# Performance work log

Hardware: AMD Instinct MI355X
Metric: run time of the kernel (lower is better)

## Reference

```python
import jax, jax.numpy as jnp
import numpy as np

B, C, N = 4, 256, 2048
H = 8
HD = C // H  # head_dim = 32


def setup_inputs() -> dict:
    key = jax.random.key(0)
    ks = jax.random.split(key, 5)
    s = 1.0 / np.sqrt(C)
    return {
        "x": jax.random.normal(ks[0], (B, C, 3, N), dtype=jnp.float32),
        "Wq": jax.random.normal(ks[1], (C, C), dtype=jnp.float32) * s,
        "Wk": jax.random.normal(ks[2], (C, C), dtype=jnp.float32) * s,
        "Wv": jax.random.normal(ks[3], (C, C), dtype=jnp.float32) * s,
        "Wo": jax.random.normal(ks[4], (C, C), dtype=jnp.float32) * s,
    }


def _vn_linear(W, x):
    # nn.Linear over channel axis: out[b,o,d,n] = sum_c W[o,c] x[b,c,d,n]
    return jnp.einsum('oc,bcdn->bodn', W, x)


def _heads(t):
    # [B,C,3,N] -> [B,H,N,HD,3]
    return t.reshape(B, H, HD, 3, N).transpose(0, 1, 4, 2, 3)


def reference(x, Wq, Wk, Wv, Wo):
    q = _heads(_vn_linear(Wq, x))
    k = _heads(_vn_linear(Wk, x))
    v = _heads(_vn_linear(Wv, x))
    # energy contracts over (head_dim, 3)
    energy = jnp.einsum('bhnci,bhmci->bhnm', q, k)
    attn = jax.nn.softmax(energy / np.sqrt(HD), axis=-1)
    out = jnp.einsum('bhnm,bhmci->bhnci', attn, v)
    # [B,H,N,HD,3] -> [B,C,3,N]
    out = out.transpose(0, 1, 3, 4, 2).reshape(B, C, 3, N)
    out = _vn_linear(Wo, out)
    return out + x
```

## Files before the change

kernel.cpp:

```cpp
#include <hip/hip_runtime.h>
#include <hip/hip_bf16.h>
#include <cmath>


typedef unsigned short u16;
typedef unsigned int   u32;
typedef u16   u16x8  __attribute__((ext_vector_type(8)));
typedef short s16x8  __attribute__((ext_vector_type(8)));
typedef float f32x4  __attribute__((ext_vector_type(4)));
typedef float f32x16 __attribute__((ext_vector_type(16)));

namespace {
constexpr int Nc = 2048, Fc = 96;
constexpr float SCALE_LOG2 = 0.17677669529663687f * 1.4426950408889634f;
constexpr int KP = 104;
constexpr int VP = 40;
constexpr int VOFF = 32 * KP;
constexpr int SBUF = VOFF + 96 * VP;
}

__device__ inline float fast_exp2(float x) {
#if __has_builtin(__builtin_amdgcn_exp2f)
    return __builtin_amdgcn_exp2f(x);
#else
    return exp2f(x);
#endif
}

__device__ inline u16 f2bf(float x) {
    union { float f; unsigned u; } v; v.f = x;
    unsigned r = v.u + 0x7FFFu + ((v.u >> 16) & 1u);
    return (u16)(r >> 16);
}

__device__ inline float bf2f(u16 x) {
    union { unsigned u; float f; } v; v.u = ((unsigned)x) << 16; return v.f;
}

__global__ __launch_bounds__(256) void wconv_kernel(
    const float* __restrict__ Wq, const float* __restrict__ Wk,
    const float* __restrict__ Wv, const float* __restrict__ Wo,
    u16* __restrict__ Wb)
{
    const int id = blockIdx.x * 256 + threadIdx.x;
    const int base = id * 8;
    const int o = base >> 8, c = base & 255;
    const int sel = o >> 8, ol = o & 255;
    const float* src = (sel == 0) ? Wq : (sel == 1) ? Wk : (sel == 2) ? Wv : Wo;
    const float sc = (sel == 0) ? SCALE_LOG2 : 1.0f;
    const float4 a = *(const float4*)&src[(size_t)ol * 256 + c];
    const float4 b = *(const float4*)&src[(size_t)ol * 256 + c + 4];
    u16x8 r;
    r[0]=f2bf(a.x*sc); r[1]=f2bf(a.y*sc); r[2]=f2bf(a.z*sc); r[3]=f2bf(a.w*sc);
    r[4]=f2bf(b.x*sc); r[5]=f2bf(b.y*sc); r[6]=f2bf(b.z*sc); r[7]=f2bf(b.w*sc);
    *(u16x8*)&Wb[(size_t)o * 256 + c] = r;
}

__global__ __launch_bounds__(256) void xt_kernel(
    const float* __restrict__ x, u16* __restrict__ xt)
{
    const int nt = blockIdx.x, ct = blockIdx.y, bi = blockIdx.z;
    const int b = bi / 3, i = bi % 3;
    const int t = (int)threadIdx.x;
    const int n0 = nt * 64, c0 = ct * 64;

    __shared__ u16 tile[64][72];

    const int n_l = t & 63;
#pragma unroll
    for (int it = 0; it < 16; ++it) {
        const int c_l = (t >> 6) + it * 4;
        tile[n_l][c_l] =
            f2bf(x[(((size_t)(b * 256 + c0 + c_l)) * 3 + i) * Nc + n0 + n_l]);
    }
    __syncthreads();
#pragma unroll
    for (int it = 0; it < 2; ++it) {
        const int idx = t + it * 256;
        const int nn = idx >> 3, part = idx & 7;
        *(u16x8*)&xt[((size_t)bi * Nc + n0 + nn) * 256 + c0 + part * 8] =
            *(const u16x8*)&tile[nn][part * 8];
    }
}

__global__ __launch_bounds__(256) void qkv_gemm_kernel(
    const u16* __restrict__ xt, const u16* __restrict__ wb,
    u16* __restrict__ Qt, u16* __restrict__ Kt, u16* __restrict__ Vf)
{
    const int nt = blockIdx.x;
    const int wy = blockIdx.y;
    const int bi = blockIdx.z;
    const int b = bi / 3, i = bi % 3;
    const int wsel = wy >> 1, ot = wy & 1;

    const u16* xs = xt + ((size_t)bi * Nc + nt * 128) * 256;
    const u16* ws = wb + (size_t)(wsel * 256 + ot * 128) * 256;

    __shared__ u16 xl[128][40];
    __shared__ u16 wl[128][40];

    const int t = (int)threadIdx.x;
    const int wv = t >> 6, lane = t & 63;
    const int g = lane >> 4, c16 = lane & 15;
    const int wr = wv >> 1, wc = wv & 1;

    f32x4 acc[4][4];
#pragma unroll
    for (int mi = 0; mi < 4; ++mi)
#pragma unroll
        for (int ni = 0; ni < 4; ++ni)
#pragma unroll
            for (int r = 0; r < 4; ++r) acc[mi][ni][r] = 0.f;

    for (int ks = 0; ks < 8; ++ks) {
        __syncthreads();
#pragma unroll
        for (int it = 0; it < 2; ++it) {
            const int idx = t + it * 256;
            const int row = idx >> 2, part = idx & 3;
            *(u16x8*)&xl[row][part * 8] =
                *(const u16x8*)&xs[(size_t)row * 256 + ks * 32 + part * 8];
            *(u16x8*)&wl[row][part * 8] =
                *(const u16x8*)&ws[(size_t)row * 256 + ks * 32 + part * 8];
        }
        __syncthreads();

        s16x8 af[4], bf[4];
        if (wsel < 2) {
#pragma unroll
            for (int mi = 0; mi < 4; ++mi) af[mi] = *(const s16x8*)&xl[wr*64 + mi*16 + c16][g*8];
#pragma unroll
            for (int ni = 0; ni < 4; ++ni) bf[ni] = *(const s16x8*)&wl[wc*64 + ni*16 + c16][g*8];
        } else {
#pragma unroll
            for (int mi = 0; mi < 4; ++mi) af[mi] = *(const s16x8*)&wl[wr*64 + mi*16 + c16][g*8];
#pragma unroll
            for (int ni = 0; ni < 4; ++ni) bf[ni] = *(const s16x8*)&xl[wc*64 + ni*16 + c16][g*8];
        }
#pragma unroll
        for (int mi = 0; mi < 4; ++mi)
#pragma unroll
            for (int ni = 0; ni < 4; ++ni)
                acc[mi][ni] = __builtin_amdgcn_mfma_f32_16x16x32_bf16(
                    af[mi], bf[ni], acc[mi][ni], 0, 0, 0);
    }

    if (wsel < 2) {
        u16* dst = wsel ? Kt : Qt;
#pragma unroll
        for (int mi = 0; mi < 4; ++mi)
#pragma unroll
            for (int ni = 0; ni < 4; ++ni) {
                const int o = ot * 128 + wc * 64 + ni * 16 + c16;
                const int h = o >> 5, cw = o & 31;
#pragma unroll
                for (int r = 0; r < 4; ++r) {
                    const int n = nt * 128 + wr * 64 + mi * 16 + g * 4 + r;
                    dst[((size_t)(b * 8 + h) * Nc + n) * Fc + i * 32 + cw] =
                        f2bf(acc[mi][ni][r]);
                }
            }
    } else {
#pragma unroll
        for (int mi = 0; mi < 4; ++mi)
#pragma unroll
            for (int ni = 0; ni < 4; ++ni) {
                const int n = nt * 128 + wc * 64 + ni * 16 + c16;
#pragma unroll
                for (int r = 0; r < 4; ++r) {
                    const int o = ot * 128 + wr * 64 + mi * 16 + g * 4 + r;
                    const int h = o >> 5, cw = o & 31;
                    Vf[((size_t)(b * 8 + h) * Fc + i * 32 + cw) * Nc + n] =
                        f2bf(acc[mi][ni][r]);
                }
            }
    }
}

__global__ __launch_bounds__(256) void attn_mfma_kernel(
    const u16* __restrict__ Qt, const u16* __restrict__ Kt,
    const u16* __restrict__ Vf, u16* __restrict__ Ob, float* __restrict__ lP)
{
    const int bid = (int)blockIdx.x;
    const int lid = (bid & 7) * 128 + (bid >> 3);
    const int bh   = lid >> 5;
    const int r5   = lid & 31;
    const int qt   = r5 >> 1;
    const int half = r5 & 1;

    const int t_   = (int)threadIdx.x;
    const int wq   = t_ >> 6;
    const int lane = t_ & 63;
    const int ql   = lane & 31;
    const int hi   = lane >> 5;

    __shared__ u16 sbuf[2 * SBUF];

    const int qb = qt * 128 + wq * 32;
    const int k0 = half * 1024;

    s16x8 bq[6];
#pragma unroll
    for (int s6 = 0; s6 < 6; ++s6)
        bq[s6] = *(const s16x8*)&Qt[((size_t)bh * Nc + qb + ql) * Fc + s6 * 16 + hi * 8];

    const u16* g_cur[3]; int g_str[3], g_dst[3];
#pragma unroll
    for (int it = 0; it < 3; ++it) {
        const int c = t_ + it * 256;
        if (c < 384) {
            const int row = c / 12, part = c - row * 12;
            g_cur[it] = Kt + ((size_t)bh * Nc + k0 + row) * Fc + part * 8;
            g_str[it] = 32 * Fc;
            g_dst[it] = row * KP + part * 8;
        } else {
            const int c2 = c - 384, f = c2 >> 2, part = c2 & 3;
            g_cur[it] = Vf + ((size_t)bh * Fc + f) * Nc + k0 + part * 8;
            g_str[it] = 32;
            g_dst[it] = VOFF + f * VP + part * 8;
        }
    }

    f32x16 acc[3];
#pragma unroll
    for (int ft = 0; ft < 3; ++ft)
#pragma unroll
        for (int r = 0; r < 16; ++r) acc[ft][r] = 0.f;
    float lacc[8];
#pragma unroll
    for (int r = 0; r < 8; ++r) lacc[r] = 0.f;

    u16* bA = sbuf;
    u16* bB = sbuf + SBUF;

    u16x8 sreg[3];
#pragma unroll
    for (int it = 0; it < 3; ++it) { sreg[it] = *(const u16x8*)g_cur[it]; g_cur[it] += g_str[it]; }
#pragma unroll
    for (int it = 0; it < 3; ++it) *(u16x8*)&bA[g_dst[it]] = sreg[it];
#pragma unroll
    for (int it = 0; it < 3; ++it) { sreg[it] = *(const u16x8*)g_cur[it]; g_cur[it] += g_str[it]; }
    __syncthreads();

    for (int kt = 0; kt < 32; ++kt) {
        if (kt < 31) {
#pragma unroll
            for (int it = 0; it < 3; ++it) *(u16x8*)&bB[g_dst[it]] = sreg[it];
        }
        if (kt < 30) {
#pragma unroll
            for (int it = 0; it < 3; ++it) { sreg[it] = *(const u16x8*)g_cur[it]; g_cur[it] += g_str[it]; }
        }

        f32x16 sv;
#pragma unroll
        for (int r = 0; r < 16; ++r) sv[r] = 0.f;
#pragma unroll
        for (int s6 = 0; s6 < 6; ++s6) {
            const s16x8 ka = *(const s16x8*)&bA[ql * KP + s6 * 16 + hi * 8];
            sv = __builtin_amdgcn_mfma_f32_32x32x16_bf16(ka, bq[s6], sv, 0, 0, 0);
        }

#pragma unroll
        for (int r = 0; r < 16; ++r) sv[r] = fast_exp2(sv[r]);
#pragma unroll
        for (int r = 0; r < 8; ++r) lacc[r] += sv[r] + sv[r + 8];

        u32 pk8[8];
#pragma unroll
        for (int j = 0; j < 8; ++j)
            asm("v_cvt_pk_bf16_f32 %0, %1, %2" : "=v"(pk8[j]) : "v"(sv[2*j]), "v"(sv[2*j+1]));
        asm volatile("v_permlane32_swap_b32 %0, %1" : "+v"(pk8[0]), "+v"(pk8[2]));
        asm volatile("v_permlane32_swap_b32 %0, %1" : "+v"(pk8[1]), "+v"(pk8[3]));
        asm volatile("v_permlane32_swap_b32 %0, %1" : "+v"(pk8[4]), "+v"(pk8[6]));
        asm volatile("v_permlane32_swap_b32 %0, %1" : "+v"(pk8[5]), "+v"(pk8[7]));
        union U { u32 w[4]; s16x8 v; } pb0, pb1;
        pb0.w[0]=pk8[0]; pb0.w[1]=pk8[1]; pb0.w[2]=pk8[2]; pb0.w[3]=pk8[3];
        pb1.w[0]=pk8[4]; pb1.w[1]=pk8[5]; pb1.w[2]=pk8[6]; pb1.w[3]=pk8[7];

#pragma unroll
        for (int ft = 0; ft < 3; ++ft) {
            const s16x8 va0 = *(const s16x8*)&bA[VOFF + (ft * 32 + ql) * VP + hi * 8];
            acc[ft] = __builtin_amdgcn_mfma_f32_32x32x16_bf16(va0, pb0.v, acc[ft], 0, 0, 0);
            const s16x8 va1 = *(const s16x8*)&bA[VOFF + (ft * 32 + ql) * VP + 16 + hi * 8];
            acc[ft] = __builtin_amdgcn_mfma_f32_32x32x16_bf16(va1, pb1.v, acc[ft], 0, 0, 0);
        }

        if (kt < 31) __syncthreads();
        { u16* tmp = bA; bA = bB; bB = tmp; }
    }

    float l4[4];
#pragma unroll
    for (int r = 0; r < 4; ++r) l4[r] = lacc[r] + lacc[r + 4];
    float l_s = (l4[0] + l4[2]) + (l4[1] + l4[3]);
    l_s += __shfl_xor(l_s, 32);
    const float inv = 1.f / l_s;

    u16* dst = Ob + (((size_t)half * 32 + bh) * Fc) * Nc;
#pragma unroll
    for (int ft = 0; ft < 3; ++ft)
#pragma unroll
        for (int r = 0; r < 16; ++r) {
            const int frow = (r & 3) + 8 * (r >> 2) + 4 * hi;
            dst[(size_t)(ft * 32 + frow) * Nc + qb + ql] = f2bf(acc[ft][r] * inv);
        }
    if (hi == 0)
        lP[((size_t)half * 32 + bh) * Nc + qb + ql] = l_s;
}

__global__ __launch_bounds__(256) void combine_kernel(
    const u16* __restrict__ Ob, const float* __restrict__ lP,
    u16* __restrict__ aot)
{
    const int nt = blockIdx.x;
    const int bh = blockIdx.y;
    const int t = (int)threadIdx.x;
    const int n0 = nt * 64;
    const int b = bh >> 3, h = bh & 7;

    __shared__ float wgt[64];
    __shared__ u16 tile[64][104];

    if (t < 64) {
        const float l0 = lP[(size_t)bh * Nc + n0 + t];
        const float l1 = lP[((size_t)32 + bh) * Nc + n0 + t];
        wgt[t] = l0 / (l0 + l1);
    }
    __syncthreads();

    const int q = t & 63;
    const int fw = t >> 6;
    const u16* p0 = Ob + ((size_t)bh * Fc) * Nc;
    const u16* p1 = Ob + (((size_t)32 + bh) * Fc) * Nc;
    const float w0 = wgt[q];
#pragma unroll
    for (int it = 0; it < 24; ++it) {
        const int f = it * 4 + fw;
        const float a0 = bf2f(p0[(size_t)f * Nc + n0 + q]);
        const float a1 = bf2f(p1[(size_t)f * Nc + n0 + q]);
        tile[q][f] = f2bf(a0 * w0 + a1 * (1.f - w0));
    }
    __syncthreads();

    const int nn = t >> 2, part = t & 3;
#pragma unroll
    for (int i = 0; i < 3; ++i) {
        *(u16x8*)&aot[((size_t)(b * 3 + i) * Nc + n0 + nn) * 256 + h * 32 + part * 8] =
            *(const u16x8*)&tile[nn][i * 32 + part * 8];
    }
}

__global__ __launch_bounds__(256) void out_gemm_kernel(
    const u16* __restrict__ aot, const u16* __restrict__ wb,
    const float* __restrict__ x, float* __restrict__ out)
{
    const int nt = blockIdx.x, ot = blockIdx.y, bi = blockIdx.z;
    const int b = bi / 3, i = bi % 3;

    const u16* bs = aot + ((size_t)bi * Nc + nt * 128) * 256;
    const u16* ws = wb + (size_t)(768 + ot * 128) * 256;

    __shared__ u16 al[128][40];
    __shared__ u16 wl[128][40];

    const int t = (int)threadIdx.x;
    const int wv = t >> 6, lane = t & 63;
    const int g = lane >> 4, c16 = lane & 15;
    const int wr = wv >> 1, wc = wv & 1;

    f32x4 acc[4][4];
#pragma unroll
    for (int mi = 0; mi < 4; ++mi)
#pragma unroll
        for (int ni = 0; ni < 4; ++ni)
#pragma unroll
            for (int r = 0; r < 4; ++r) acc[mi][ni][r] = 0.f;

    for (int ks = 0; ks < 8; ++ks) {
        __syncthreads();
#pragma unroll
        for (int it = 0; it < 2; ++it) {
            const int idx = t + it * 256;
            const int row = idx >> 2, part = idx & 3;
            *(u16x8*)&al[row][part * 8] =
                *(const u16x8*)&bs[(size_t)row * 256 + ks * 32 + part * 8];
            *(u16x8*)&wl[row][part * 8] =
                *(const u16x8*)&ws[(size_t)row * 256 + ks * 32 + part * 8];
        }
        __syncthreads();

        s16x8 af[4], bf[4];
#pragma unroll
        for (int mi = 0; mi < 4; ++mi) af[mi] = *(const s16x8*)&wl[wr*64 + mi*16 + c16][g*8];
#pragma unroll
        for (int ni = 0; ni < 4; ++ni) bf[ni] = *(const s16x8*)&al[wc*64 + ni*16 + c16][g*8];
#pragma unroll
        for (int mi = 0; mi < 4; ++mi)
#pragma unroll
            for (int ni = 0; ni < 4; ++ni)
                acc[mi][ni] = __builtin_amdgcn_mfma_f32_16x16x32_bf16(
                    af[mi], bf[ni], acc[mi][ni], 0, 0, 0);
    }

#pragma unroll
    for (int mi = 0; mi < 4; ++mi)
#pragma unroll
        for (int ni = 0; ni < 4; ++ni) {
            const int n = nt * 128 + wc * 64 + ni * 16 + c16;
#pragma unroll
            for (int r = 0; r < 4; ++r) {
                const int o = ot * 128 + wr * 64 + mi * 16 + g * 4 + r;
                const size_t idx = ((size_t)(b * 256 + o) * 3 + i) * Nc + n;
                out[idx] = x[idx] + acc[mi][ni][r];
            }
        }
}

extern "C" void kernel_launch(void* const* d_in, const int* in_sizes, int n_in,
                              void* d_out, int out_size, void* d_ws, size_t ws_size,
                              hipStream_t stream) {
    const float* x  = (const float*)d_in[0];
    const float* Wq = (const float*)d_in[1];
    const float* Wk = (const float*)d_in[2];
    const float* Wv = (const float*)d_in[3];
    const float* Wo = (const float*)d_in[4];
    float* out = (float*)d_out;

    const size_t E = (size_t)32 * Fc * Nc;
    u16* xt  = (u16*)d_ws;
    u16* wbw = xt + E;
    u16* qt  = wbw + 262144;
    u16* kt  = qt + E;
    u16* vf  = kt + E;
    u16* obp = vf + E;
    float* lP = (float*)(obp + 2 * E);
    u16* aot = xt;

    dim3 blk(256);
    wconv_kernel    <<<dim3(128),        blk, 0, stream>>>(Wq, Wk, Wv, Wo, wbw);
    xt_kernel       <<<dim3(32, 4, 12),  blk, 0, stream>>>(x, xt);
    qkv_gemm_kernel <<<dim3(16, 6, 12),  blk, 0, stream>>>(xt, wbw, qt, kt, vf);
    attn_mfma_kernel<<<dim3(1024),       blk, 0, stream>>>(qt, kt, vf, obp, lP);
    combine_kernel  <<<dim3(32, 32),     blk, 0, stream>>>(obp, lP, aot);
    out_gemm_kernel <<<dim3(16, 2, 12),  blk, 0, stream>>>(aot, wbw, x, out);
}
```

Measured before the change: 134.7 us.

## Double queries per warp in attention and fuse split-K combine into output GEMM

Each attention warp now handles 64 queries (two 32-row MFMA tiles) and shares each K/V LDS fragment across both, halving the grid and the K/V staging traffic per query. Attention partials are written through LDS in the transposed [half][b,i][n][C] layout the output GEMM consumes. The separate combine kernel is removed, and the out GEMM blends the two key-half partials using the lP weights while loading its A tile. This saves a launch and a full read/write pass over the partials. In exchange it raises register pressure in the attention kernel, lowers block count, and adds redundant lP loads and divides inside the GEMM load loop.

```diff
diff --git a/kernel.cpp b/kernel.cpp
--- a/kernel.cpp
+++ b/kernel.cpp
@@ -1,7 +1,6 @@
 #include <hip/hip_runtime.h>
 #include <hip/hip_bf16.h>
 #include <cmath>
-
 
 typedef unsigned short u16;
 typedef unsigned int   u32;
@@ -179,14 +178,14 @@
 
 __global__ __launch_bounds__(256) void attn_mfma_kernel(
     const u16* __restrict__ Qt, const u16* __restrict__ Kt,
-    const u16* __restrict__ Vf, u16* __restrict__ Ob, float* __restrict__ lP)
+    const u16* __restrict__ Vf, u16* __restrict__ obt, float* __restrict__ lP)
 {
     const int bid = (int)blockIdx.x;
-    const int lid = (bid & 7) * 128 + (bid >> 3);
-    const int bh   = lid >> 5;
-    const int r5   = lid & 31;
-    const int qt   = r5 >> 1;
-    const int half = r5 & 1;
+    const int lid = (bid & 7) * 64 + (bid >> 3);
+    const int bh   = lid >> 4;
+    const int r4   = lid & 15;
+    const int qt   = r4 >> 1;
+    const int half = r4 & 1;
 
     const int t_   = (int)threadIdx.x;
     const int wq   = t_ >> 6;
@@ -196,13 +195,15 @@
 
     __shared__ u16 sbuf[2 * SBUF];
 
-    const int qb = qt * 128 + wq * 32;
+    const int qb = qt * 256 + wq * 64;
     const int k0 = half * 1024;
 
-    s16x8 bq[6];
-#pragma unroll
-    for (int s6 = 0; s6 < 6; ++s6)
-        bq[s6] = *(const s16x8*)&Qt[((size_t)bh * Nc + qb + ql) * Fc + s6 * 16 + hi * 8];
+    s16x8 bq[2][6];
+#pragma unroll
+    for (int qs = 0; qs < 2; ++qs)
+#pragma unroll
+        for (int s6 = 0; s6 < 6; ++s6)
+            bq[qs][s6] = *(const s16x8*)&Qt[((size_t)bh * Nc + qb + qs * 32 + ql) * Fc + s6 * 16 + hi * 8];
 
     const u16* g_cur[3]; int g_str[3], g_dst[3];
 #pragma unroll
@@ -221,14 +222,18 @@
         }
     }
 
-    f32x16 acc[3];
-#pragma unroll
-    for (int ft = 0; ft < 3; ++ft)
-#pragma unroll
-        for (int r = 0; r < 16; ++r) acc[ft][r] = 0.f;
-    float lacc[8];
-#pragma unroll
-    for (int r = 0; r < 8; ++r) lacc[r] = 0.f;
+    f32x16 acc[2][3];
+#pragma unroll
+    for (int qs = 0; qs < 2; ++qs)
+#pragma unroll
+        for (int ft = 0; ft < 3; ++ft)
+#pragma unroll
+            for (int r = 0; r < 16; ++r) acc[qs][ft][r] = 0.f;
+    float lacc[2][4];
+#pragma unroll
+    for (int qs = 0; qs < 2; ++qs)
+#pragma unroll
+        for (int r = 0; r < 4; ++r) lacc[qs][r] = 0.f;
 
     u16* bA = sbuf;
     u16* bB = sbuf + SBUF;
@@ -252,113 +257,115 @@
             for (int it = 0; it < 3; ++it) { sreg[it] = *(const u16x8*)g_cur[it]; g_cur[it] += g_str[it]; }
         }
 
-        f32x16 sv;
-#pragma unroll
-        for (int r = 0; r < 16; ++r) sv[r] = 0.f;
+        f32x16 sv0, sv1;
+#pragma unroll
+        for (int r = 0; r < 16; ++r) { sv0[r] = 0.f; sv1[r] = 0.f; }
 #pragma unroll
         for (int s6 = 0; s6 < 6; ++s6) {
             const s16x8 ka = *(const s16x8*)&bA[ql * KP + s6 * 16 + hi * 8];
-            sv = __builtin_amdgcn_mfma_f32_32x32x16_bf16(ka, bq[s6], sv, 0, 0, 0);
-        }
-
-#pragma unroll
-        for (int r = 0; r < 16; ++r) sv[r] = fast_exp2(sv[r]);
-#pragma unroll
-        for (int r = 0; r < 8; ++r) lacc[r] += sv[r] + sv[r + 8];
-
-        u32 pk8[8];
-#pragma unroll
-        for (int j = 0; j < 8; ++j)
-            asm("v_cvt_pk_bf16_f32 %0, %1, %2" : "=v"(pk8[j]) : "v"(sv[2*j]), "v"(sv[2*j+1]));
-        asm volatile("v_permlane32_swap_b32 %0, %1" : "+v"(pk8[0]), "+v"(pk8[2]));
-        asm volatile("v_permlane32_swap_b32 %0, %1" : "+v"(pk8[1]), "+v"(pk8[3]));
-        asm volatile("v_permlane32_swap_b32 %0, %1" : "+v"(pk8[4]), "+v"(pk8[6]));
-        asm volatile("v_permlane32_swap_b32 %0, %1" : "+v"(pk8[5]), "+v"(pk8[7]));
-        union U { u32 w[4]; s16x8 v; } pb0, pb1;
-        pb0.w[0]=pk8[0]; pb0.w[1]=pk8[1]; pb0.w[2]=pk8[2]; pb0.w[3]=pk8[3];
-        pb1.w[0]=pk8[4]; pb1.w[1]=pk8[5]; pb1.w[2]=pk8[6]; pb1.w[3]=pk8[7];
+            sv0 = __builtin_amdgcn_mfma_f32_32x32x16_bf16(ka, bq[0][s6], sv0, 0, 0, 0);
+            sv1 = __builtin_amdgcn_mfma_f32_32x32x16_bf16(ka, bq[1][s6], sv1, 0, 0, 0);
+        }
+
+#pragma unroll
+        for (int r = 0; r < 16; ++r) { sv0[r] = fast_exp2(sv0[r]); sv1[r] = fast_exp2(sv1[r]); }
+#pragma unroll
+        for (int r = 0; r < 4; ++r) {
+            lacc[0][r] += (sv0[r] + sv0[r + 8]) + (sv0[r + 4] + sv0[r + 12]);
+            lacc[1][r] += (sv1[r] + sv1[r + 8]) + (sv1[r + 4] + sv1[r + 12]);
+        }
+
+        union U { u32 w[4]; s16x8 v; } pb[2][2];
+#pragma unroll
+        for (int qs = 0; qs < 2; ++qs) {
+            const f32x16& sv = qs ? sv1 : sv0;
+            u32 pk8[8];
+#pragma unroll
+            for (int j = 0; j < 8; ++j)
+                asm("v_cvt_pk_bf16_f32 %0, %1, %2" : "=v"(pk8[j]) : "v"(sv[2*j]), "v"(sv[2*j+1]));
+            asm volatile("v_permlane32_swap_b32 %0, %1" : "+v"(pk8[0]), "+v"(pk8[2]));
+            asm volatile("v_permlane32_swap_b32 %0, %1" : "+v"(pk8[1]), "+v"(pk8[3]));
+            asm volatile("v_permlane32_swap_b32 %0, %1" : "+v"(pk8[4]), "+v"(pk8[6]));
+            asm volatile("v_permlane32_swap_b32 %0, %1" : "+v"(pk8[5]), "+v"(pk8[7]));
+            pb[qs][0].w[0]=pk8[0]; pb[qs][0].w[1]=pk8[1]; pb[qs][0].w[2]=pk8[2]; pb[qs][0].w[3]=pk8[3];
+            pb[qs][1].w[0]=pk8[4]; pb[qs][1].w[1]=pk8[5]; pb[qs][1].w[2]=pk8[6]; pb[qs][1].w[3]=pk8[7];
+        }
 
 #pragma unroll
         for (int ft = 0; ft < 3; ++ft) {
             const s16x8 va0 = *(const s16x8*)&bA[VOFF + (ft * 32 + ql) * VP + hi * 8];
-            acc[ft] = __builtin_amdgcn_mfma_f32_32x32x16_bf16(va0, pb0.v, acc[ft], 0, 0, 0);
+            acc[0][ft] = __builtin_amdgcn_mfma_f32_32x32x16_bf16(va0, pb[0][0].v, acc[0][ft], 0, 0, 0);
+            acc[1][ft] = __builtin_amdgcn_mfma_f32_32x32x16_bf16(va0, pb[1][0].v, acc[1][ft], 0, 0, 0);
             const s16x8 va1 = *(const s16x8*)&bA[VOFF + (ft * 32 + ql) * VP + 16 + hi * 8];
-            acc[ft] = __builtin_amdgcn_mfma_f32_32x32x16_bf16(va1, pb1.v, acc[ft], 0, 0, 0);
+            acc[0][ft] = __builtin_amdgcn_mfma_f32_32x32x16_bf16(va1, pb[0][1].v, acc[0][ft], 0, 0, 0);
+            acc[1][ft] = __builtin_amdgcn_mfma_f32_32x32x16_bf16(va1, pb[1][1].v, acc[1][ft], 0, 0, 0);
         }
 
         if (kt < 31) __syncthreads();
         { u16* tmp = bA; bA = bB; bB = tmp; }
     }
 
-    float l4[4];
-#pragma unroll
-    for (int r = 0; r < 4; ++r) l4[r] = lacc[r] + lacc[r + 4];
-    float l_s = (l4[0] + l4[2]) + (l4[1] + l4[3]);
-    l_s += __shfl_xor(l_s, 32);
-    const float inv = 1.f / l_s;
-
-    u16* dst = Ob + (((size_t)half * 32 + bh) * Fc) * Nc;
-#pragma unroll
-    for (int ft = 0; ft < 3; ++ft)
-#pragma unroll
-        for (int r = 0; r < 16; ++r) {
-            const int frow = (r & 3) + 8 * (r >> 2) + 4 * hi;
-            dst[(size_t)(ft * 32 + frow) * Nc + qb + ql] = f2bf(acc[ft][r] * inv);
-        }
-    if (hi == 0)
-        lP[((size_t)half * 32 + bh) * Nc + qb + ql] = l_s;
-}
-
-__global__ __launch_bounds__(256) void combine_kernel(
-    const u16* __restrict__ Ob, const float* __restrict__ lP,
-    u16* __restrict__ aot)
-{
-    const int nt = blockIdx.x;
-    const int bh = blockIdx.y;
-    const int t = (int)threadIdx.x;
-    const int n0 = nt * 64;
-    const int b = bh >> 3, h = bh & 7;
-
-    __shared__ float wgt[64];
-    __shared__ u16 tile[64][104];
-
-    if (t < 64) {
-        const float l0 = lP[(size_t)bh * Nc + n0 + t];
-        const float l1 = lP[((size_t)32 + bh) * Nc + n0 + t];
-        wgt[t] = l0 / (l0 + l1);
-    }
-    __syncthreads();
-
-    const int q = t & 63;
-    const int fw = t >> 6;
-    const u16* p0 = Ob + ((size_t)bh * Fc) * Nc;
-    const u16* p1 = Ob + (((size_t)32 + bh) * Fc) * Nc;
-    const float w0 = wgt[q];
-#pragma unroll
-    for (int it = 0; it < 24; ++it) {
-        const int f = it * 4 + fw;
-        const float a0 = bf2f(p0[(size_t)f * Nc + n0 + q]);
-        const float a1 = bf2f(p1[(size_t)f * Nc + n0 + q]);
-        tile[q][f] = f2bf(a0 * w0 + a1 * (1.f - w0));
-    }
-    __syncthreads();
-
-    const int nn = t >> 2, part = t & 3;
-#pragma unroll
-    for (int i = 0; i < 3; ++i) {
-        *(u16x8*)&aot[((size_t)(b * 3 + i) * Nc + n0 + nn) * 256 + h * 32 + part * 8] =
-            *(const u16x8*)&tile[nn][i * 32 + part * 8];
+    float inv[2];
+#pragma unroll
+    for (int qs = 0; qs < 2; ++qs) {
+        float l_s = (lacc[qs][0] + lacc[qs][2]) + (lacc[qs][1] + lacc[qs][3]);
+        l_s += __shfl_xor(l_s, 32);
+        inv[qs] = 1.f / l_s;
+        if (hi == 0)
+            lP[((size_t)half * 32 + bh) * Nc + qb + qs * 32 + ql] = l_s;
+    }
+
+    const int b_ = bh >> 3, h_ = bh & 7;
+    u16* ot = sbuf + wq * 3328;
+#pragma unroll
+    for (int qs = 0; qs < 2; ++qs) {
+        __syncthreads();
+#pragma unroll
+        for (int ft = 0; ft < 3; ++ft)
+#pragma unroll
+            for (int r = 0; r < 16; ++r) {
+                const int frow = (r & 3) + 8 * (r >> 2) + 4 * hi;
+                ot[ql * 104 + ft * 32 + frow] = f2bf(acc[qs][ft][r] * inv[qs]);
+            }
+        __syncthreads();
+
+        u16x8 v6[6];
+#pragma unroll
+        for (int j = 0; j < 6; ++j)
+            v6[j] = *(const u16x8*)&ot[ql * 104 + hi * 48 + j * 8];
+
+        const int n = qb + qs * 32 + ql;
+        const size_t base0 = (((size_t)half * 12 + b_ * 3 + 0) * Nc + n) * 256 + h_ * 32;
+        const size_t base1 = (((size_t)half * 12 + b_ * 3 + 1) * Nc + n) * 256 + h_ * 32;
+        const size_t base2 = (((size_t)half * 12 + b_ * 3 + 2) * Nc + n) * 256 + h_ * 32;
+        if (hi == 0) {
+            *(u16x8*)&obt[base0 +  0] = v6[0];
+            *(u16x8*)&obt[base0 +  8] = v6[1];
+            *(u16x8*)&obt[base0 + 16] = v6[2];
+            *(u16x8*)&obt[base0 + 24] = v6[3];
+            *(u16x8*)&obt[base1 +  0] = v6[4];
+            *(u16x8*)&obt[base1 +  8] = v6[5];
+        } else {
+            *(u16x8*)&obt[base1 + 16] = v6[0];
+            *(u16x8*)&obt[base1 + 24] = v6[1];
+            *(u16x8*)&obt[base2 +  0] = v6[2];
+            *(u16x8*)&obt[base2 +  8] = v6[3];
+            *(u16x8*)&obt[base2 + 16] = v6[4];
+            *(u16x8*)&obt[base2 + 24] = v6[5];
+        }
     }
 }
 
 __global__ __launch_bounds__(256) void out_gemm_kernel(
-    const u16* __restrict__ aot, const u16* __restrict__ wb,
-    const float* __restrict__ x, float* __restrict__ out)
+    const u16* __restrict__ obt, const float* __restrict__ lP,
+    const u16* __restrict__ wb, const float* __restrict__ x,
+    float* __restrict__ out)
 {
     const int nt = blockIdx.x, ot = blockIdx.y, bi = blockIdx.z;
     const int b = bi / 3, i = bi % 3;
 
-    const u16* bs = aot + ((size_t)bi * Nc + nt * 128) * 256;
+    const u16* p0 = obt + ((size_t)bi * Nc) * 256;
+    const u16* p1 = obt + (((size_t)12 + bi) * Nc) * 256;
     const u16* ws = wb + (size_t)(768 + ot * 128) * 256;
 
     __shared__ u16 al[128][40];
@@ -383,8 +390,18 @@
         for (int it = 0; it < 2; ++it) {
             const int idx = t + it * 256;
             const int row = idx >> 2, part = idx & 3;
-            *(u16x8*)&al[row][part * 8] =
-                *(const u16x8*)&bs[(size_t)row * 256 + ks * 32 + part * 8];
+            const int n = nt * 128 + row;
+            const float l0 = lP[((size_t)(b * 8 + ks)) * Nc + n];
+            const float l1 = lP[((size_t)(32 + b * 8 + ks)) * Nc + n];
+            const float w0 = l0 / (l0 + l1);
+            const float w1 = 1.f - w0;
+            const u16x8 a0 = *(const u16x8*)&p0[(size_t)n * 256 + ks * 32 + part * 8];
+            const u16x8 a1 = *(const u16x8*)&p1[(size_t)n * 256 + ks * 32 + part * 8];
+            u16x8 rr;
+#pragma unroll
+            for (int j = 0; j < 8; ++j)
+                rr[j] = f2bf(bf2f(a0[j]) * w0 + bf2f(a1[j]) * w1);
+            *(u16x8*)&al[row][part * 8] = rr;
             *(u16x8*)&wl[row][part * 8] =
                 *(const u16x8*)&ws[(size_t)row * 256 + ks * 32 + part * 8];
         }
@@ -433,15 +450,13 @@
     u16* qt  = wbw + 262144;
     u16* kt  = qt + E;
     u16* vf  = kt + E;
-    u16* obp = vf + E;
-    float* lP = (float*)(obp + 2 * E);
-    u16* aot = xt;
+    u16* obt = vf + E;
+    float* lP = (float*)(obt + 2 * E);
 
     dim3 blk(256);
     wconv_kernel    <<<dim3(128),        blk, 0, stream>>>(Wq, Wk, Wv, Wo, wbw);
     xt_kernel       <<<dim3(32, 4, 12),  blk, 0, stream>>>(x, xt);
     qkv_gemm_kernel <<<dim3(16, 6, 12),  blk, 0, stream>>>(xt, wbw, qt, kt, vf);
-    attn_mfma_kernel<<<dim3(1024),       blk, 0, stream>>>(qt, kt, vf, obp, lP);
-    combine_kernel  <<<dim3(32, 32),     blk, 0, stream>>>(obp, lP, aot);
-    out_gemm_kernel <<<dim3(16, 2, 12),  blk, 0, stream>>>(aot, wbw, x, out);
-}
+    attn_mfma_kernel<<<dim3(512),        blk, 0, stream>>>(qt, kt, vf, obt, lP);
+    out_gemm_kernel <<<dim3(16, 2, 12),  blk, 0, stream>>>(obt, lP, wbw, x, out);
+}
```

Measured after the change: 126.3 us. 6.2% less time.
